# Kernel optimization log

Hardware: AMD Instinct MI355X
Metric: run time of the kernel (lower is better)

The kernel has to match this reference:

```python
import jax, jax.numpy as jnp
import numpy as np

EPS = 1e-6  # torch.pairwise_distance default eps

def _linear(x, w, b):
    return x @ w.T + b

def _patch_attend(x, patches):
    # x: [B, C]; patches: [B, C, S]
    # torch.pairwise_distance(x.view(B,C,1), patches) -> [B, S] (norm over C)
    d = jnp.sqrt(jnp.sum((x[:, :, None] - patches + EPS) ** 2, axis=1))  # [B,S]
    p = jax.nn.softmax(jnp.exp(-d), axis=1)                              # [B,S]
    return jnp.einsum('bcs,bs->bc', patches, p)                          # [B,C]

def _get_D_and_A_m(HSI_D, LiDAR_D, data_HSI, data_LiDAR, m, K,
                   w1a, b1a, w2a, b2a):
    # Reconstructed get_D_and_A_m: cross-attention between batch features and
    # dictionary atoms using the attention net, with momentum dictionary update.
    # HSI_D, LiDAR_D: [30, D_num] (transposed dictionaries); data_*: [B, 30]
    # attention: H1 = lin1(H); D1 = lin2(D.T).T; H2 = lin1(H).T; D2 = lin2(D.T)
    H1_h = _linear(data_HSI, w1a, b1a)          # [B,60]
    D2_h = _linear(HSI_D.T, w2a, b2a)           # [D_num,60]
    S_h = H1_h @ D2_h.T                          # [B, D_num]
    A_h = jax.nn.softmax(S_h, axis=1)            # [B, D_num]
    out_h = A_h @ HSI_D.T                        # [B, 30]
    newD_h = m * HSI_D + (1.0 - m) * (data_HSI.T @ A_h)  # [30, D_num]

    H1_l = _linear(data_LiDAR, w1a, b1a)
    D2_l = _linear(LiDAR_D.T, w2a, b2a)
    S_l = H1_l @ D2_l.T
    A_l = jax.nn.softmax(S_l, axis=1)
    out_l = A_l @ LiDAR_D.T
    newD_l = m * LiDAR_D + (1.0 - m) * (data_LiDAR.T @ A_l)

    # A returned transposed ([60?]) -- model does HSI_A = HSI_A.T then cat dim=1
    # and out expects 120 features => A here must be [60, B]-like. We project
    # attended output through lin1 to get 60-dim features, transpose for return.
    feat_h = _linear(out_h, w1a, b1a).T          # [60, B]
    feat_l = _linear(out_l, w1a, b1a).T          # [60, B]
    return out_h, feat_h, newD_h, out_l, feat_l, newD_l

def setup_inputs():
    key = jax.random.key(0)
    ks = jax.random.split(key, 24)
    f = jax.random.normal
    inp = {
        'H_HSI': f(ks[0], (16384, 63), jnp.float32),
        'H_LiDAR': f(ks[1], (16384, 1), jnp.float32),
        'HSI_D': f(ks[2], (64, 63), jnp.float32),
        'LiDAR_D': f(ks[3], (64, 1), jnp.float32),
        'Patch_HSI': f(ks[4], (16384, 63, 49), jnp.float32),
        'Patch_LiDAR': f(ks[5], (16384, 1, 49), jnp.float32),
        'D_Patch_HSI': f(ks[6], (64, 63, 49), jnp.float32),
        'D_Patch_LiDAR': f(ks[7], (64, 1, 49), jnp.float32),
        'K': 10, 'm': 1, 'batchsize': 16384, 'D_num': 64,
    }
    def lin(k, o, i):
        k1, k2 = jax.random.split(k)
        s = 1.0 / np.sqrt(i)
        return (jax.random.uniform(k1, (o, i), jnp.float32, -s, s),
                jax.random.uniform(k2, (o,), jnp.float32, -s, s))
    inp['w1_1'], inp['b1_1'] = lin(ks[8], 45, 63)
    inp['w1_2'], inp['b1_2'] = lin(ks[9], 30, 45)
    inp['w2_1'], inp['b2_1'] = lin(ks[10], 15, 1)
    inp['w2_2'], inp['b2_2'] = lin(ks[11], 30, 15)
    inp['wa1'], inp['ba1'] = lin(ks[12], 60, 30)
    inp['wa2'], inp['ba2'] = lin(ks[13], 60, 30)
    inp['wo1'], inp['bo1'] = lin(ks[14], 60, 120)
    inp['wo2'], inp['bo2'] = lin(ks[15], 7, 60)
    return inp

def reference(H_HSI, H_LiDAR, HSI_D, LiDAR_D, Patch_HSI, Patch_LiDAR,
              D_Patch_HSI, D_Patch_LiDAR, K, m, batchsize, D_num,
              w1_1, b1_1, w1_2, b1_2, w2_1, b2_1, w2_2, b2_2,
              wa1, ba1, wa2, ba2, wo1, bo1, wo2, bo2):
    # patch attention aggregation for each branch
    SP_HSI = _patch_attend(H_HSI.reshape(H_HSI.shape[0], -1), Patch_HSI)
    SP_LiDAR = _patch_attend(H_LiDAR.reshape(H_LiDAR.shape[0], -1), Patch_LiDAR)
    D_SP_HSI = _patch_attend(HSI_D.reshape(HSI_D.shape[0], -1), D_Patch_HSI)
    D_SP_LiDAR = _patch_attend(LiDAR_D.reshape(LiDAR_D.shape[0], -1), D_Patch_LiDAR)

    lin1 = lambda x: _linear(_linear(x, w1_1, b1_1), w1_2, b1_2)  # 63->30
    lin2 = lambda x: _linear(_linear(x, w2_1, b2_1), w2_2, b2_2)  # 1->30

    data_HSI = lin1(SP_HSI)          # [B,30]
    data_LiDAR = lin2(SP_LiDAR)      # [B,30]
    HSI_Dp = lin1(D_SP_HSI).T        # [30,D_num]
    LiDAR_Dp = lin2(D_SP_LiDAR).T    # [30,D_num]

    mf = jnp.float32(m)
    out_h, HSI_A, HSI_Dn, out_l, LiDAR_A, LiDAR_Dn = _get_D_and_A_m(
        HSI_Dp, LiDAR_Dp, data_HSI, data_LiDAR, mf, K, wa1, ba1, wa2, ba2)

    HSI_A = HSI_A.T      # [B,60]
    LiDAR_A = LiDAR_A.T  # [B,60]
    A = jnp.concatenate([LiDAR_A, HSI_A], axis=1)  # [B,120]
    output = _linear(_linear(A, wo1, bo1), wo2, bo2)  # [B,Classes]
    return (data_HSI, data_LiDAR, HSI_A, HSI_Dn, LiDAR_A, LiDAR_Dn, output)
```

## Files before the change

kernel.cpp:

```cpp
#include <hip/hip_runtime.h>
#include <math.h>

#define NB 16384
#define DN 64
#define ST 68
#define OFF1 491520
#define OFF2 983040
#define OFF3 1966080
#define OFF4 1968000
#define OFF5 2951040
#define OFF6 2952960
#define SPH_OFF  0
#define SPL_OFF  1048576
#define DSPH_OFF 1064960
#define DSPL_OFF 1069056
#define DPTH_OFF 1069120
#define DPTL_OFF 1071040
#define D2H_OFF  1072960
#define D2L_OFF  1076800
#define AH_OFF   1080640
#define AL_OFF   2129216

typedef const __attribute__((address_space(1))) void* gas_ptr;
typedef __attribute__((address_space(3))) void* las_ptr;

__device__ __forceinline__ float wredmax(float v) {
#pragma unroll
    for (int m = 32; m; m >>= 1) v = fmaxf(v, __shfl_xor(v, m, 64));
    return v;
}
__device__ __forceinline__ float wredsum(float v) {
#pragma unroll
    for (int m = 32; m; m >>= 1) v += __shfl_xor(v, m, 64);
    return v;
}

template<int CH>
__device__ __forceinline__ void load_chunk(const float* __restrict__ xrow, float* __restrict__ x) {
    const int NQ = CH >> 2;
#pragma unroll
    for (int q = 0; q < NQ; ++q) {
        float4 v = *(const float4*)(xrow + 4 * q);
        x[4 * q] = v.x; x[4 * q + 1] = v.y; x[4 * q + 2] = v.z; x[4 * q + 3] = v.w;
    }
#pragma unroll
    for (int j = NQ * 4; j < CH; ++j) x[j] = xrow[j];
}

template<int INS, int RS, int PER>
__device__ __forceinline__ void dlayer4(const float* __restrict__ W,
                                        const float* __restrict__ bias,
                                        const float* __restrict__ xb,
                                        float* __restrict__ yb,
                                        const int OUTS, const int o0,
                                        const float scale)
{
    float acc[PER];
#pragma unroll
    for (int k = 0; k < PER; ++k) {
        int oc = o0 + k; oc = oc < OUTS ? oc : OUTS - 1;
        acc[k] = bias ? bias[oc] : 0.0f;
    }
#pragma unroll
    for (int c0 = 0; c0 < INS; c0 += 16) {
        const int CHv = (INS - c0) < 16 ? (INS - c0) : 16;
        float x[16];
        if (CHv == 16) load_chunk<16>(xb + c0, x);
        else if (CHv == 15) load_chunk<15>(xb + c0, x);
        else if (CHv == 14) load_chunk<14>(xb + c0, x);
        else if (CHv == 13) load_chunk<13>(xb + c0, x);
        else if (CHv == 12) load_chunk<12>(xb + c0, x);
        else {
#pragma unroll
            for (int j = 0; j < 16; ++j) if (j < CHv) x[j] = xb[c0 + j];
        }
#pragma unroll
        for (int k = 0; k < PER; ++k) {
            int oc = o0 + k; oc = oc < OUTS ? oc : OUTS - 1;
            const float* Wr = W + oc * RS + c0;
            float a = acc[k];
#pragma unroll
            for (int j = 0; j < 16; ++j) if (j < CHv) a = fmaf(Wr[j], x[j], a);
            acc[k] = a;
        }
    }
#pragma unroll
    for (int k = 0; k < PER; ++k) {
        int o = o0 + k;
        if (o < OUTS) yb[o] = acc[k] * scale;
    }
}

template<int INS, int CS, int PER>
__device__ __forceinline__ void dlayerT4(const float* __restrict__ W,
                                         const float* __restrict__ xb,
                                         float* __restrict__ yb,
                                         const int OUTS, const int o0,
                                         const float scale)
{
    float acc[PER];
#pragma unroll
    for (int k = 0; k < PER; ++k) acc[k] = 0.0f;
#pragma unroll
    for (int c0 = 0; c0 < INS; c0 += 16) {
        float x[16];
        load_chunk<16>(xb + c0, x);
#pragma unroll
        for (int j = 0; j < 16; ++j) {
            const float* Wr = W + (c0 + j) * CS + o0;
#pragma unroll
            for (int k = 0; k < PER; ++k) acc[k] = fmaf(Wr[k], x[j], acc[k]);
        }
    }
#pragma unroll
    for (int k = 0; k < PER; ++k) {
        int o = o0 + k;
        if (o < OUTS) yb[o] = acc[k] * scale;
    }
}

__device__ __forceinline__ void softmax_exp8(const float* __restrict__ Sb,
                                             float* __restrict__ Qb,
                                             float* __restrict__ P,
                                             const int wb, const int l)
{
    const float4* S4 = (const float4*)Sb;
    float4 m4 = S4[0];
#pragma unroll
    for (int q = 1; q < 16; ++q) {
        float4 v = S4[q];
        m4.x = fmaxf(m4.x, v.x); m4.y = fmaxf(m4.y, v.y);
        m4.z = fmaxf(m4.z, v.z); m4.w = fmaxf(m4.w, v.w);
    }
    const float mx = fmaxf(fmaxf(m4.x, m4.y), fmaxf(m4.z, m4.w));
    float4 a = S4[2 * wb], bq = S4[2 * wb + 1];
    float4 ea, eb;
    ea.x = __expf(a.x - mx); ea.y = __expf(a.y - mx);
    ea.z = __expf(a.z - mx); ea.w = __expf(a.w - mx);
    eb.x = __expf(bq.x - mx); eb.y = __expf(bq.y - mx);
    eb.z = __expf(bq.z - mx); eb.w = __expf(bq.w - mx);
    ((float4*)Qb)[2 * wb] = ea;
    ((float4*)Qb)[2 * wb + 1] = eb;
    P[wb * 64 + l] = ((ea.x + ea.y) + (ea.z + ea.w)) + ((eb.x + eb.y) + (eb.z + eb.w));
}

__device__ __forceinline__ float inv8(const float* __restrict__ P, const int l)
{
    float s0 = P[l] + P[64 + l], s1 = P[128 + l] + P[192 + l];
    float s2 = P[256 + l] + P[320 + l], s3 = P[384 + l] + P[448 + l];
    return 1.0f / ((s0 + s1) + (s2 + s3));
}

__global__ __launch_bounds__(256) void patch_attend_kernel(
    const float* __restrict__ patchH, const float* __restrict__ xH,
    const float* __restrict__ patchL, const float* __restrict__ xL,
    float* __restrict__ spH, float* __restrict__ spL,
    const float* __restrict__ dpH, const float* __restrict__ dxH,
    const float* __restrict__ dpL, const float* __restrict__ dxL,
    float* __restrict__ dspH, float* __restrict__ dspL)
{
    __shared__ __align__(16) float ph[4 * 3087];
    __shared__ __align__(16) float pl_[4 * 49];
    __shared__ __align__(16) float xh[4 * 63];
    __shared__ float xls[4];
    __shared__ float pw[4 * 49];

    const int tid = threadIdx.x;
    const bool isD = blockIdx.x >= (NB / 4);
    const int b0 = (isD ? (blockIdx.x - NB / 4) : blockIdx.x) * 4;
    const float* PH = isD ? dpH : patchH;
    const float* XH = isD ? dxH : xH;
    const float* PL = isD ? dpL : patchL;
    const float* XL = isD ? dxL : xL;
    float* SH = isD ? dspH : spH;
    float* SL = isD ? dspL : spL;
    {
        const float4* s4 = (const float4*)(PH + (size_t)b0 * 3087);
        float4* d4 = (float4*)ph;
        for (int i = tid; i < 3087; i += 256) {
            __builtin_amdgcn_global_load_lds((gas_ptr)(const void*)(s4 + i),
                                             (las_ptr)(void*)(d4 + i), 16, 0, 0);
        }
        if (tid < 49) ((float4*)pl_)[tid] = ((const float4*)(PL + (size_t)b0 * 49))[tid];
        if (tid >= 64 && tid < 127) ((float4*)xh)[tid - 64] = ((const float4*)(XH + (size_t)b0 * 63))[tid - 64];
        if (tid == 255) *((float4*)xls) = *((const float4*)(XL + b0));
    }
    asm volatile("s_waitcnt vmcnt(0)" ::: "memory");
    __syncthreads();

    const int w = tid >> 6, l = tid & 63;
    const float* phw = ph + w * 3087;
    const float* plw = pl_ + w * 49;
    const float* xhw = xh + w * 63;
    const float xlw = xls[w];

    float eh = -INFINITY, el = -INFINITY;
    if (l < 49) {
        float acc = 0.f;
#pragma unroll
        for (int c = 0; c < 63; ++c) {
            float t = xhw[c] - phw[c * 49 + l] + 1e-6f;
            acc = fmaf(t, t, acc);
        }
        eh = __expf(-sqrtf(acc));
        float tl = xlw - plw[l] + 1e-6f;
        el = __expf(-fabsf(tl));
    }
    float mh = wredmax(eh), ml = wredmax(el);
    float qh = (l < 49) ? __expf(eh - mh) : 0.f;
    float ql = (l < 49) ? __expf(el - ml) : 0.f;
    float sh = wredsum(qh);
    float sl = wredsum(ql);
    if (l < 49) pw[w * 49 + l] = qh / sh;
    float spl_v = wredsum((l < 49) ? plw[l] * (ql / sl) : 0.f);
    if (l == 0) SL[b0 + w] = spl_v;
    __syncthreads();
    if (l < 63) {
        float acc = 0.f;
        const float* pww = pw + w * 49;
#pragma unroll
        for (int s = 0; s < 49; ++s) acc = fmaf(phw[l * 49 + s], pww[s], acc);
        SH[(size_t)(b0 + w) * 64 + l] = acc;
    }
}

__global__ __launch_bounds__(1024) void dict_chain_kernel(
    const float* __restrict__ dsph, const float* __restrict__ dspl,
    const float* __restrict__ w1_1, const float* __restrict__ b1_1,
    const float* __restrict__ w1_2, const float* __restrict__ b1_2,
    const float* __restrict__ w2_1, const float* __restrict__ b2_1,
    const float* __restrict__ w2_2, const float* __restrict__ b2_2,
    const float* __restrict__ wa2, const float* __restrict__ ba2,
    float* __restrict__ dptH, float* __restrict__ dptL,
    float* __restrict__ d2H, float* __restrict__ d2L,
    const int* __restrict__ mI, float* __restrict__ out)
{
    __shared__ __align__(16) float HA[64 * ST];
    __shared__ __align__(16) float HB[64 * ST];
    __shared__ __align__(16) float LA[64 * ST];
    __shared__ __align__(16) float LB[64 * ST];
    __shared__ float XLs[64];
    const int tid = threadIdx.x;
    const int w = __builtin_amdgcn_readfirstlane(tid >> 6);
    const int wb = w & 7;
    const bool isH = w < 8;
    const int l = tid & 63;
    const float mf = (float)(*mI);
    {
        int r = tid >> 4, q = tid & 15;
        *(float4*)(HA + r * ST + 4 * q) = ((const float4*)dsph)[tid];
        if (tid < 64) XLs[tid] = dspl[tid];
    }
    __syncthreads();
    if (isH) {
        dlayer4<63, 63, 6>(w1_1, b1_1, HA + l * ST, HB + l * ST, 45, wb * 6, 1.0f);
    } else {
        const float xl = XLs[l];
#pragma unroll
        for (int k = 0; k < 2; ++k) {
            int o = wb * 2 + k;
            if (o < 15) LB[l * ST + o] = fmaf(w2_1[o], xl, b2_1[o]);
        }
    }
    __syncthreads();
    if (isH) dlayer4<45, 45, 4>(w1_2, b1_2, HB + l * ST, HA + l * ST, 30, wb * 4, 1.0f);
    else     dlayer4<15, 15, 4>(w2_2, b2_2, LB + l * ST, LA + l * ST, 30, wb * 4, 1.0f);
    __syncthreads();
    for (int i = tid; i < 1920; i += 1024) {
        int r = i / 30, c = i - r * 30;
        dptH[i] = HA[r * ST + c];
        dptL[i] = LA[r * ST + c];
    }
    for (int i = tid; i < 1920; i += 1024) {
        int c = i >> 6, j = i & 63;
        out[OFF3 + i] = mf * HA[j * ST + c];
        out[OFF5 + i] = mf * LA[j * ST + c];
    }
    if (isH) dlayer4<30, 30, 8>(wa2, ba2, HA + l * ST, HB + l * ST, 60, wb * 8, 1.0f);
    else     dlayer4<30, 30, 8>(wa2, ba2, LA + l * ST, LB + l * ST, 60, wb * 8, 1.0f);
    __syncthreads();
    for (int i = tid; i < 3840; i += 1024) {
        int r = i / 60, c = i - r * 60;
        d2H[i] = HB[r * ST + c];
        d2L[i] = LB[r * ST + c];
    }
}

__global__ __launch_bounds__(1024) void chain_kernel(
    const float* __restrict__ spH, const float* __restrict__ spL,
    const float* __restrict__ dptH, const float* __restrict__ dptL,
    const float* __restrict__ d2H, const float* __restrict__ d2L,
    const float* __restrict__ w1_1, const float* __restrict__ b1_1,
    const float* __restrict__ w1_2, const float* __restrict__ b1_2,
    const float* __restrict__ w2_1, const float* __restrict__ b2_1,
    const float* __restrict__ w2_2, const float* __restrict__ b2_2,
    const float* __restrict__ wa1, const float* __restrict__ ba1,
    const float* __restrict__ wo1, const float* __restrict__ bo1,
    const float* __restrict__ wo2, const float* __restrict__ bo2,
    const int* __restrict__ mI,
    float* __restrict__ out, float* __restrict__ aH, float* __restrict__ aL)
{
    __shared__ __align__(16) float HA[64 * ST];
    __shared__ __align__(16) float HB[64 * ST];
    __shared__ __align__(16) float LA[64 * ST];
    __shared__ __align__(16) float LB[64 * ST];
    __shared__ float XLs[64];
    __shared__ float PH[8 * 64], PL[8 * 64];

    const int tid = threadIdx.x;
    const int w = __builtin_amdgcn_readfirstlane(tid >> 6);
    const int wb = w & 7;
    const bool isH = w < 8;
    const int l = tid & 63;
    const int b0 = blockIdx.x * 64;
    const int b = b0 + l;
    const float mf = (float)(*mI);

    {
        int r = tid >> 4, q = tid & 15;
        *(float4*)(HA + r * ST + 4 * q) = ((const float4*)(spH + (size_t)b0 * 64))[tid];
        if (tid < 64) XLs[tid] = spL[b0 + tid];
    }
    __syncthreads();
    if (isH) {
        dlayer4<63, 63, 6>(w1_1, b1_1, HA + l * ST, HB + l * ST, 45, wb * 6, 1.0f);
    } else {
        const float xl = XLs[l];
#pragma unroll
        for (int k = 0; k < 2; ++k) {
            int o = wb * 2 + k;
            if (o < 15) LB[l * ST + o] = fmaf(w2_1[o], xl, b2_1[o]);
        }
    }
    __syncthreads();
    if (isH) dlayer4<45, 45, 4>(w1_2, b1_2, HB + l * ST, HA + l * ST, 30, wb * 4, 1.0f);
    else     dlayer4<15, 15, 4>(w2_2, b2_2, LB + l * ST, LA + l * ST, 30, wb * 4, 1.0f);
    __syncthreads();
    for (int i = tid; i < 1920; i += 1024) {
        int r = i / 30, c = i - r * 30;
        out[(size_t)b0 * 30 + i] = HA[r * ST + c];
        out[OFF1 + (size_t)b0 * 30 + i] = LA[r * ST + c];
    }
    if (isH) dlayer4<30, 30, 8>(wa1, ba1, HA + l * ST, HB + l * ST, 60, wb * 8, 1.0f);
    else     dlayer4<30, 30, 8>(wa1, ba1, LA + l * ST, LB + l * ST, 60, wb * 8, 1.0f);
    __syncthreads();
    if (isH) dlayer4<60, 60, 8>(d2H, nullptr, HB + l * ST, HA + l * ST, 64, wb * 8, 1.0f);
    else     dlayer4<60, 60, 8>(d2L, nullptr, LB + l * ST, LA + l * ST, 64, wb * 8, 1.0f);
    __syncthreads();
    if (isH) softmax_exp8(HA + l * ST, HB + l * ST, PH, wb, l);
    else     softmax_exp8(LA + l * ST, LB + l * ST, PL, wb, l);
    __syncthreads();
    if (mf != 1.0f) {
        if (isH) {
            for (int i = tid; i < 4096; i += 512) {
                int r = i >> 6, j = i & 63;
                aH[(size_t)b0 * 64 + i] = HB[r * ST + j] * inv8(PH, r);
            }
        } else {
            for (int i = tid - 512; i < 4096; i += 512) {
                int r = i >> 6, j = i & 63;
                aL[(size_t)b0 * 64 + i] = LB[r * ST + j] * inv8(PL, r);
            }
        }
    }
    if (isH) dlayerT4<64, 30, 4>(dptH, HB + l * ST, HA + l * ST, 30, wb * 4, inv8(PH, l));
    else     dlayerT4<64, 30, 4>(dptL, LB + l * ST, LA + l * ST, 30, wb * 4, inv8(PL, l));
    __syncthreads();
    if (isH) dlayer4<30, 30, 8>(wa1, ba1, HA + l * ST, HB + l * ST, 60, wb * 8, 1.0f);
    else     dlayer4<30, 30, 8>(wa1, ba1, LA + l * ST, LB + l * ST, 60, wb * 8, 1.0f);
    __syncthreads();
    for (int i = tid; i < 3840; i += 1024) {
        int r = i / 60, c = i - r * 60;
        out[OFF2 + (size_t)b0 * 60 + i] = HB[r * ST + c];
        out[OFF4 + (size_t)b0 * 60 + i] = LB[r * ST + c];
    }
    {
        const int o0 = w * 4;
        float acc[4];
#pragma unroll
        for (int k = 0; k < 4; ++k) acc[k] = (o0 + k < 60) ? bo1[o0 + k] : 0.0f;
#pragma unroll
        for (int c0 = 0; c0 < 60; c0 += 16) {
            const int CH = (60 - c0) < 16 ? (60 - c0) : 16;
            float x[16];
            if (CH == 16) load_chunk<16>(LB + l * ST + c0, x);
            else load_chunk<12>(LB + l * ST + c0, x);
#pragma unroll
            for (int k = 0; k < 4; ++k) {
                int oc = o0 + k; oc = oc < 60 ? oc : 59;
                const float* Wr = wo1 + oc * 120 + c0;
                float a = acc[k];
#pragma unroll
                for (int j = 0; j < 16; ++j) if (j < CH) a = fmaf(Wr[j], x[j], a);
                acc[k] = a;
            }
        }
#pragma unroll
        for (int c0 = 0; c0 < 60; c0 += 16) {
            const int CH = (60 - c0) < 16 ? (60 - c0) : 16;
            float x[16];
            if (CH == 16) load_chunk<16>(HB + l * ST + c0, x);
            else load_chunk<12>(HB + l * ST + c0, x);
#pragma unroll
            for (int k = 0; k < 4; ++k) {
                int oc = o0 + k; oc = oc < 60 ? oc : 59;
                const float* Wr = wo1 + oc * 120 + 60 + c0;
                float a = acc[k];
#pragma unroll
                for (int j = 0; j < 16; ++j) if (j < CH) a = fmaf(Wr[j], x[j], a);
                acc[k] = a;
            }
        }
        if (o0 < 60) {
            float4 av; av.x = acc[0]; av.y = acc[1]; av.z = acc[2]; av.w = acc[3];
            *((float4*)(HA + l * ST + o0)) = av;
        }
    }
    __syncthreads();
    if (w < 7) {
        float a = bo2[w];
        const float* Wr = wo2 + w * 60;
#pragma unroll
        for (int c0 = 0; c0 < 60; c0 += 16) {
            const int CH = (60 - c0) < 16 ? (60 - c0) : 16;
            float x[16];
            if (CH == 16) load_chunk<16>(HA + l * ST + c0, x);
            else load_chunk<12>(HA + l * ST + c0, x);
#pragma unroll
            for (int j = 0; j < 16; ++j) if (j < CH) a = fmaf(Wr[c0 + j], x[j], a);
        }
        out[OFF6 + (size_t)b * 7 + w] = a;
    }
}

__global__ __launch_bounds__(256) void momentum_kernel(
    const float* __restrict__ dataH, const float* __restrict__ dataL,
    const float* __restrict__ aH, const float* __restrict__ aL,
    const int* __restrict__ mI, float* __restrict__ out)
{
    const float mf = (float)(*mI);
    if (mf == 1.0f) return;
    const int tid = threadIdx.x;
    const int chunk = blockIdx.x & 63;
    const int mod = blockIdx.x >> 6;
    const float* data = mod ? dataL : dataH;
    const float* A = mod ? aL : aH;
    float* D = out + (mod ? OFF5 : OFF3);
    const int b0 = chunk * 256;
    const int j = tid & 63;
    const int g = tid >> 6;
    float acc[8];
#pragma unroll
    for (int k = 0; k < 8; ++k) acc[k] = 0.f;
    for (int bb = 0; bb < 256; ++bb) {
        float a = A[(size_t)(b0 + bb) * 64 + j];
#pragma unroll
        for (int k = 0; k < 8; ++k) {
            int c = g + 4 * k; c = c < 30 ? c : 29;
            acc[k] = fmaf(data[(size_t)(b0 + bb) * 30 + c], a, acc[k]);
        }
    }
    const float s = 1.0f - mf;
#pragma unroll
    for (int k = 0; k < 8; ++k) {
        int c = g + 4 * k;
        if (c < 30) atomicAdd(&D[c * 64 + j], s * acc[k]);
    }
}

extern "C" void kernel_launch(void* const* d_in, const int* in_sizes, int n_in,
                              void* d_out, int out_size, void* d_ws, size_t ws_size,
                              hipStream_t stream) {
    const float* H_HSI        = (const float*)d_in[0];
    const float* H_LiDAR      = (const float*)d_in[1];
    const float* HSI_D        = (const float*)d_in[2];
    const float* LiDAR_D      = (const float*)d_in[3];
    const float* Patch_HSI    = (const float*)d_in[4];
    const float* Patch_LiDAR  = (const float*)d_in[5];
    const float* D_Patch_HSI  = (const float*)d_in[6];
    const float* D_Patch_LiDAR= (const float*)d_in[7];
    const int*   mI           = (const int*)d_in[9];
    const float* w1_1 = (const float*)d_in[12];
    const float* b1_1 = (const float*)d_in[13];
    const float* w1_2 = (const float*)d_in[14];
    const float* b1_2 = (const float*)d_in[15];
    const float* w2_1 = (const float*)d_in[16];
    const float* b2_1 = (const float*)d_in[17];
    const float* w2_2 = (const float*)d_in[18];
    const float* b2_2 = (const float*)d_in[19];
    const float* wa1  = (const float*)d_in[20];
    const float* ba1  = (const float*)d_in[21];
    const float* wa2  = (const float*)d_in[22];
    const float* ba2  = (const float*)d_in[23];
    const float* wo1  = (const float*)d_in[24];
    const float* bo1  = (const float*)d_in[25];
    const float* wo2  = (const float*)d_in[26];
    const float* bo2  = (const float*)d_in[27];

    float* out = (float*)d_out;
    float* ws  = (float*)d_ws;

    patch_attend_kernel<<<NB / 4 + DN / 4, 256, 0, stream>>>(
        Patch_HSI, H_HSI, Patch_LiDAR, H_LiDAR, ws + SPH_OFF, ws + SPL_OFF,
        D_Patch_HSI, HSI_D, D_Patch_LiDAR, LiDAR_D, ws + DSPH_OFF, ws + DSPL_OFF);
    dict_chain_kernel<<<1, 1024, 0, stream>>>(
        ws + DSPH_OFF, ws + DSPL_OFF,
        w1_1, b1_1, w1_2, b1_2, w2_1, b2_1, w2_2, b2_2, wa2, ba2,
        ws + DPTH_OFF, ws + DPTL_OFF, ws + D2H_OFF, ws + D2L_OFF, mI, out);
    chain_kernel<<<NB / 64, 1024, 0, stream>>>(
        ws + SPH_OFF, ws + SPL_OFF,
        ws + DPTH_OFF, ws + DPTL_OFF, ws + D2H_OFF, ws + D2L_OFF,
        w1_1, b1_1, w1_2, b1_2, w2_1, b2_1, w2_2, b2_2,
        wa1, ba1, wo1, bo1, wo2, bo2, mI,
        out, ws + AH_OFF, ws + AL_OFF);
    momentum_kernel<<<128, 256, 0, stream>>>(
        out, out + OFF1, ws + AH_OFF, ws + AL_OFF, mI, out);
}
```

Baseline: 99.10 us.

## Split each layer across all 16 waves for both branches instead of per-branch halves

```diff
diff --git a/kernel.cpp b/kernel.cpp
--- a/kernel.cpp
+++ b/kernel.cpp
@@ -119,10 +119,10 @@
     }
 }
 
-__device__ __forceinline__ void softmax_exp8(const float* __restrict__ Sb,
+__device__ __forceinline__ void softmax_exp4(const float* __restrict__ Sb,
                                              float* __restrict__ Qb,
                                              float* __restrict__ P,
-                                             const int wb, const int l)
+                                             const int w, const int l)
 {
     const float4* S4 = (const float4*)Sb;
     float4 m4 = S4[0];
@@ -133,21 +133,24 @@
         m4.z = fmaxf(m4.z, v.z); m4.w = fmaxf(m4.w, v.w);
     }
     const float mx = fmaxf(fmaxf(m4.x, m4.y), fmaxf(m4.z, m4.w));
-    float4 a = S4[2 * wb], bq = S4[2 * wb + 1];
-    float4 ea, eb;
-    ea.x = __expf(a.x - mx); ea.y = __expf(a.y - mx);
-    ea.z = __expf(a.z - mx); ea.w = __expf(a.w - mx);
-    eb.x = __expf(bq.x - mx); eb.y = __expf(bq.y - mx);
-    eb.z = __expf(bq.z - mx); eb.w = __expf(bq.w - mx);
-    ((float4*)Qb)[2 * wb] = ea;
-    ((float4*)Qb)[2 * wb + 1] = eb;
-    P[wb * 64 + l] = ((ea.x + ea.y) + (ea.z + ea.w)) + ((eb.x + eb.y) + (eb.z + eb.w));
-}
-
-__device__ __forceinline__ float inv8(const float* __restrict__ P, const int l)
-{
-    float s0 = P[l] + P[64 + l], s1 = P[128 + l] + P[192 + l];
-    float s2 = P[256 + l] + P[320 + l], s3 = P[384 + l] + P[448 + l];
+    float4 sv = S4[w];
+    float4 e;
+    e.x = __expf(sv.x - mx); e.y = __expf(sv.y - mx);
+    e.z = __expf(sv.z - mx); e.w = __expf(sv.w - mx);
+    ((float4*)Qb)[w] = e;
+    P[w * 64 + l] = (e.x + e.y) + (e.z + e.w);
+}
+
+__device__ __forceinline__ float inv16(const float* __restrict__ P, const int l)
+{
+    float s0 = P[l], s1 = P[64 + l], s2 = P[128 + l], s3 = P[192 + l];
+#pragma unroll
+    for (int g = 4; g < 16; g += 4) {
+        s0 += P[g * 64 + l];
+        s1 += P[(g + 1) * 64 + l];
+        s2 += P[(g + 2) * 64 + l];
+        s3 += P[(g + 3) * 64 + l];
+    }
     return 1.0f / ((s0 + s1) + (s2 + s3));
 }
 
@@ -242,8 +245,6 @@
     __shared__ float XLs[64];
     const int tid = threadIdx.x;
     const int w = __builtin_amdgcn_readfirstlane(tid >> 6);
-    const int wb = w & 7;
-    const bool isH = w < 8;
     const int l = tid & 63;
     const float mf = (float)(*mI);
     {
@@ -252,37 +253,29 @@
         if (tid < 64) XLs[tid] = dspl[tid];
     }
     __syncthreads();
-    if (isH) {
-        dlayer4<63, 63, 6>(w1_1, b1_1, HA + l * ST, HB + l * ST, 45, wb * 6, 1.0f);
-    } else {
-        const float xl = XLs[l];
-#pragma unroll
-        for (int k = 0; k < 2; ++k) {
-            int o = wb * 2 + k;
-            if (o < 15) LB[l * ST + o] = fmaf(w2_1[o], xl, b2_1[o]);
-        }
-    }
-    __syncthreads();
-    if (isH) dlayer4<45, 45, 4>(w1_2, b1_2, HB + l * ST, HA + l * ST, 30, wb * 4, 1.0f);
-    else     dlayer4<15, 15, 4>(w2_2, b2_2, LB + l * ST, LA + l * ST, 30, wb * 4, 1.0f);
+    dlayer4<63, 63, 3>(w1_1, b1_1, HA + l * ST, HB + l * ST, 45, w * 3, 1.0f);
+    dlayer4<1, 1, 1>(w2_1, b2_1, XLs + l, LA + l * ST, 15, w, 1.0f);
+    __syncthreads();
+    dlayer4<45, 45, 2>(w1_2, b1_2, HB + l * ST, HA + l * ST, 30, w * 2, 1.0f);
+    dlayer4<15, 15, 2>(w2_2, b2_2, LA + l * ST, LB + l * ST, 30, w * 2, 1.0f);
     __syncthreads();
     for (int i = tid; i < 1920; i += 1024) {
         int r = i / 30, c = i - r * 30;
         dptH[i] = HA[r * ST + c];
-        dptL[i] = LA[r * ST + c];
+        dptL[i] = LB[r * ST + c];
     }
     for (int i = tid; i < 1920; i += 1024) {
         int c = i >> 6, j = i & 63;
         out[OFF3 + i] = mf * HA[j * ST + c];
-        out[OFF5 + i] = mf * LA[j * ST + c];
-    }
-    if (isH) dlayer4<30, 30, 8>(wa2, ba2, HA + l * ST, HB + l * ST, 60, wb * 8, 1.0f);
-    else     dlayer4<30, 30, 8>(wa2, ba2, LA + l * ST, LB + l * ST, 60, wb * 8, 1.0f);
+        out[OFF5 + i] = mf * LB[j * ST + c];
+    }
+    dlayer4<30, 30, 4>(wa2, ba2, HA + l * ST, HB + l * ST, 60, w * 4, 1.0f);
+    dlayer4<30, 30, 4>(wa2, ba2, LB + l * ST, LA + l * ST, 60, w * 4, 1.0f);
     __syncthreads();
     for (int i = tid; i < 3840; i += 1024) {
         int r = i / 60, c = i - r * 60;
         d2H[i] = HB[r * ST + c];
-        d2L[i] = LB[r * ST + c];
+        d2L[i] = LA[r * ST + c];
     }
 }
 
@@ -305,12 +298,10 @@
     __shared__ __align__(16) float LA[64 * ST];
     __shared__ __align__(16) float LB[64 * ST];
     __shared__ float XLs[64];
-    __shared__ float PH[8 * 64], PL[8 * 64];
+    __shared__ float PH[16 * 64], PL[16 * 64];
 
     const int tid = threadIdx.x;
     const int w = __builtin_amdgcn_readfirstlane(tid >> 6);
-    const int wb = w & 7;
-    const bool isH = w < 8;
     const int l = tid & 63;
     const int b0 = blockIdx.x * 64;
     const int b = b0 + l;
@@ -322,57 +313,48 @@
         if (tid < 64) XLs[tid] = spL[b0 + tid];
     }
     __syncthreads();
-    if (isH) {
-        dlayer4<63, 63, 6>(w1_1, b1_1, HA + l * ST, HB + l * ST, 45, wb * 6, 1.0f);
-    } else {
-        const float xl = XLs[l];
-#pragma unroll
-        for (int k = 0; k < 2; ++k) {
-            int o = wb * 2 + k;
-            if (o < 15) LB[l * ST + o] = fmaf(w2_1[o], xl, b2_1[o]);
-        }
-    }
-    __syncthreads();
-    if (isH) dlayer4<45, 45, 4>(w1_2, b1_2, HB + l * ST, HA + l * ST, 30, wb * 4, 1.0f);
-    else     dlayer4<15, 15, 4>(w2_2, b2_2, LB + l * ST, LA + l * ST, 30, wb * 4, 1.0f);
+
+    dlayer4<63, 63, 3>(w1_1, b1_1, HA + l * ST, HB + l * ST, 45, w * 3, 1.0f);
+    dlayer4<1, 1, 1>(w2_1, b2_1, XLs + l, LA + l * ST, 15, w, 1.0f);
+    __syncthreads();
+    dlayer4<45, 45, 2>(w1_2, b1_2, HB + l * ST, HA + l * ST, 30, w * 2, 1.0f);
+    dlayer4<15, 15, 2>(w2_2, b2_2, LA + l * ST, LB + l * ST, 30, w * 2, 1.0f);
     __syncthreads();
     for (int i = tid; i < 1920; i += 1024) {
         int r = i / 30, c = i - r * 30;
         out[(size_t)b0 * 30 + i] = HA[r * ST + c];
-        out[OFF1 + (size_t)b0 * 30 + i] = LA[r * ST + c];
-    }
-    if (isH) dlayer4<30, 30, 8>(wa1, ba1, HA + l * ST, HB + l * ST, 60, wb * 8, 1.0f);
-    else     dlayer4<30, 30, 8>(wa1, ba1, LA + l * ST, LB + l * ST, 60, wb * 8, 1.0f);
-    __syncthreads();
-    if (isH) dlayer4<60, 60, 8>(d2H, nullptr, HB + l * ST, HA + l * ST, 64, wb * 8, 1.0f);
-    else     dlayer4<60, 60, 8>(d2L, nullptr, LB + l * ST, LA + l * ST, 64, wb * 8, 1.0f);
-    __syncthreads();
-    if (isH) softmax_exp8(HA + l * ST, HB + l * ST, PH, wb, l);
-    else     softmax_exp8(LA + l * ST, LB + l * ST, PL, wb, l);
+        out[OFF1 + (size_t)b0 * 30 + i] = LB[r * ST + c];
+    }
+    dlayer4<30, 30, 4>(wa1, ba1, HA + l * ST, HB + l * ST, 60, w * 4, 1.0f);
+    dlayer4<30, 30, 4>(wa1, ba1, LB + l * ST, LA + l * ST, 60, w * 4, 1.0f);
+    __syncthreads();
+    dlayer4<60, 60, 4>(d2H, nullptr, HB + l * ST, HA + l * ST, 64, w * 4, 1.0f);
+    dlayer4<60, 60, 4>(d2L, nullptr, LA + l * ST, LB + l * ST, 64, w * 4, 1.0f);
+    __syncthreads();
+    softmax_exp4(HA + l * ST, HB + l * ST, PH, w, l);
+    softmax_exp4(LB + l * ST, LA + l * ST, PL, w, l);
     __syncthreads();
     if (mf != 1.0f) {
-        if (isH) {
-            for (int i = tid; i < 4096; i += 512) {
-                int r = i >> 6, j = i & 63;
-                aH[(size_t)b0 * 64 + i] = HB[r * ST + j] * inv8(PH, r);
-            }
-        } else {
-            for (int i = tid - 512; i < 4096; i += 512) {
-                int r = i >> 6, j = i & 63;
-                aL[(size_t)b0 * 64 + i] = LB[r * ST + j] * inv8(PL, r);
-            }
-        }
-    }
-    if (isH) dlayerT4<64, 30, 4>(dptH, HB + l * ST, HA + l * ST, 30, wb * 4, inv8(PH, l));
-    else     dlayerT4<64, 30, 4>(dptL, LB + l * ST, LA + l * ST, 30, wb * 4, inv8(PL, l));
-    __syncthreads();
-    if (isH) dlayer4<30, 30, 8>(wa1, ba1, HA + l * ST, HB + l * ST, 60, wb * 8, 1.0f);
-    else     dlayer4<30, 30, 8>(wa1, ba1, LA + l * ST, LB + l * ST, 60, wb * 8, 1.0f);
+        for (int i = tid; i < 4096; i += 1024) {
+            int r = i >> 6, j = i & 63;
+            aH[(size_t)b0 * 64 + i] = HB[r * ST + j] * inv16(PH, r);
+            aL[(size_t)b0 * 64 + i] = LA[r * ST + j] * inv16(PL, r);
+        }
+    }
+    {
+        const float invH = inv16(PH, l);
+        const float invL = inv16(PL, l);
+        dlayerT4<64, 30, 2>(dptH, HB + l * ST, HA + l * ST, 30, w * 2, invH);
+        dlayerT4<64, 30, 2>(dptL, LA + l * ST, LB + l * ST, 30, w * 2, invL);
+    }
+    __syncthreads();
+    dlayer4<30, 30, 4>(wa1, ba1, HA + l * ST, HB + l * ST, 60, w * 4, 1.0f);
+    dlayer4<30, 30, 4>(wa1, ba1, LB + l * ST, LA + l * ST, 60, w * 4, 1.0f);
     __syncthreads();
     for (int i = tid; i < 3840; i += 1024) {
         int r = i / 60, c = i - r * 60;
         out[OFF2 + (size_t)b0 * 60 + i] = HB[r * ST + c];
-        out[OFF4 + (size_t)b0 * 60 + i] = LB[r * ST + c];
+        out[OFF4 + (size_t)b0 * 60 + i] = LA[r * ST + c];
     }
     {
         const int o0 = w * 4;
@@ -383,8 +365,8 @@
         for (int c0 = 0; c0 < 60; c0 += 16) {
             const int CH = (60 - c0) < 16 ? (60 - c0) : 16;
             float x[16];
-            if (CH == 16) load_chunk<16>(LB + l * ST + c0, x);
-            else load_chunk<12>(LB + l * ST + c0, x);
+            if (CH == 16) load_chunk<16>(LA + l * ST + c0, x);
+            else load_chunk<12>(LA + l * ST + c0, x);
 #pragma unroll
             for (int k = 0; k < 4; ++k) {
                 int oc = o0 + k; oc = oc < 60 ? oc : 59;
```

New measurement: 84.49 us (median of 2 runs). -14.7%, faster.
